# Optimization experiments

Measured on AMD Instinct MI355X. Metric: run time of the kernel, lower is better.

## Reference

```python
import jax, jax.numpy as jnp
import numpy as np
from jax import lax

# ---- config (mirrors init_kwargs) ----
B, CIN, T, WIDTH = 32, 8, 256, 128
COUT = 64
K = (5, 5)
PAD = (2, 2)            # ceil((k-1)*dilation/2) per dim
OUT_W = 128             # output_shape
EPS = 1e-8
BETA0 = 0.9             # beta 'constant' init, one_per_layer
B0 = 1.0                # b 'constant' init
SIGMA0 = 10.0
MAX_SPK = 3.0           # Max_spikes_per_run


@jax.custom_vjp
def spike_fn(mthr, sigma):
    # Surrogate Heaviside: hard threshold fwd, sigmoid-derivative surrogate bwd.
    return (mthr > 0).astype(mthr.dtype)

def _spike_fwd(mthr, sigma):
    return spike_fn(mthr, sigma), (mthr, sigma)

def _spike_bwd(res, g):
    mthr, sigma = res
    sg = jax.nn.sigmoid(sigma * mthr)
    return (g * sigma * sg * (1.0 - sg), jnp.zeros_like(sigma))

spike_fn.defvjp(_spike_fwd, _spike_bwd)


def setup_inputs() -> dict:
    key = jax.random.key(0)
    kx, kw = jax.random.split(key)
    x = jax.random.normal(kx, (B, CIN, T, WIDTH), dtype=jnp.float32)
    w_std = 1.0 * np.sqrt(1.0 / (CIN * K[0] * K[1]))
    w = jax.random.normal(kw, (COUT, CIN, K[0], K[1]), dtype=jnp.float32) * w_std
    b = jnp.full((COUT,), B0, dtype=jnp.float32)          # clamped >= 0
    beta = jnp.array([BETA0], dtype=jnp.float32)           # one_per_layer, clamped to [0,1]
    sigma = jnp.array([SIGMA0], dtype=jnp.float32)         # surrogate_sigma_mode 'one'
    return {"x": x, "w": w, "b": b, "beta": beta, "sigma": sigma}


def _forward(x, w, b, beta, sigma):
    # conv over (time, width) with 'same'-style padding, then truncate width
    conv_x = lax.conv_general_dilated(
        x, w, window_strides=(1, 1),
        padding=((PAD[0], PAD[0]), (PAD[1], PAD[1])),
        rhs_dilation=(1, 1),
        dimension_numbers=("NCHW", "OIHW", "NCHW"))
    conv_x = conv_x[:, :, :, :OUT_W]                      # [B, COUT, T, OUT_W]

    d = jnp.einsum("oikl,eikl->oe", w, w)                 # lateral matrix [COUT, COUT]
    norm = jnp.sum(w * w, axis=(1, 2, 3))                 # [COUT]
    inv_norm = 1.0 / (norm + EPS)
    beta_s = beta[0]

    conv_seq = jnp.transpose(conv_x, (2, 0, 1, 3))        # [T, B, COUT, OUT_W]

    def step(carry, inp_t):
        mem, spk, prev = carry
        rst = jnp.einsum("bcw,cd->bdw", spk, d)           # lateral reset
        # Leaky neuron, soft reset
        mem = (mem - rst) * beta_s + inp_t * (1.0 - beta_s)
        mthr = mem * inv_norm[None, :, None] - b[None, :, None]
        s = (MAX_SPK - prev) * spike_fn(mthr, sigma)      # spike_limit=True
        prev = prev + s
        return (mem, s, prev), s

    zeros = jnp.zeros((B, COUT, OUT_W), dtype=x.dtype)
    (_, _, _), spk_rec = lax.scan(step, (zeros, zeros, zeros), conv_seq)
    # spk_rec: [T, B, COUT, OUT_W]

    loss = 0.5 * jnp.mean(spk_rec ** 2)                   # 'squared'
    spk_spread = jnp.max(jnp.sum(spk_rec, axis=(1, 2, 3))) / (B * COUT * OUT_W)  # 'max'

    output = jnp.transpose(spk_rec, (1, 2, 0, 3))         # [B, COUT, T, OUT_W]
    return output, loss, spk_spread


def reference(x, w, b, beta, sigma):
    return _forward(x, w, b, beta, sigma)
```

## Files before the change

### kernel.cpp

```cpp
#include <hip/hip_runtime.h>
#include <cstdint>


#define NB 32
#define NC 8
#define NT 256
#define NW 128
#define NO 64
#define WT 16
#define TC 8
#define NROWS 12
#define NCHUNK (NT / TC)
#define WPITCH 324

__global__ __launch_bounds__(1024)
void prep_kernel(const float* __restrict__ w, float* __restrict__ d3,
                 float* __restrict__ invn, unsigned int* __restrict__ gfires)
{
    __shared__ float wsh[NO * 200];
    const int tid = threadIdx.x;
    for (int i = tid; i < NO * 200; i += 1024) wsh[i] = w[i];
    if (tid < NT) gfires[tid] = 0u;
    __syncthreads();
#pragma unroll
    for (int p = 0; p < 4; ++p) {
        int idx = p * 1024 + tid;
        int o = idx >> 6, e = idx & 63;
        float acc = 0.0f;
        for (int i = 0; i < 200; i += 4) {
            float4 av = *(const float4*)&wsh[o * 200 + i];
            float4 bv = *(const float4*)&wsh[e * 200 + i];
            acc += av.x * bv.x + av.y * bv.y + av.z * bv.z + av.w * bv.w;
        }
        d3[idx] = 3.0f * acc;
        if (o == e) invn[o] = 1.0f / (acc + 1e-8f);
    }
}

__global__ __launch_bounds__(256, 1)
void spk_kernel(const float* __restrict__ x, const float* __restrict__ wglob,
                const float* __restrict__ bias, const float* __restrict__ beta_p,
                const float* __restrict__ d3g, const float* __restrict__ invng,
                float* __restrict__ out, unsigned int* __restrict__ gfires)
{
    __shared__ float wsm[NO * WPITCH];
    __shared__ float d3s[NO * NO];
    __shared__ float xsh[NC][NROWS][20];
    __shared__ unsigned long long smask[3][WT];
    __shared__ unsigned int scnt[3];
    __shared__ unsigned int sfires[NT];

    const int tid = threadIdx.x;
    const int bb  = blockIdx.x >> 3;
    const int w0  = (blockIdx.x & 7) * WT;
    const int co  = tid >> 2;
    const int wq4 = (tid & 3) * 4;

    for (int i = tid; i < NO * 200; i += 256) {
        int oi = i / 200; int r = i - oi * 200; int g = r / 5; int kw = r - g * 5;
        wsm[oi * WPITCH + g * 8 + kw] = wglob[i];
    }
    for (int i = tid; i < NO * NO; i += 256) d3s[i] = d3g[i];
    if (tid < WT) { smask[0][tid] = 0ull; smask[1][tid] = 0ull; smask[2][tid] = 0ull; }
    if (tid < 3) scnt[tid] = 0u;
    sfires[tid] = 0u;

    const size_t xbbase = (size_t)bb * NC * NT * NW;
#pragma unroll
    for (int k = 0; k < 8; ++k) {
        int i = tid + k * 256;
        if (i < NC * NROWS * 20) {
            int c = i / (NROWS * 20); int rem = i - c * (NROWS * 20);
            int row = rem / 20; int col = rem - row * 20;
            int tg = row - 2; int wg = w0 + col - 2;
            float v = 0.0f;
            if (tg >= 0 && tg < NT && wg >= 0 && wg < NW)
                v = x[xbbase + ((size_t)c * NT + tg) * NW + wg];
            ((float*)xsh)[i] = v;
        }
    }

    const float invn = invng[co];
    const float bco  = bias[co];
    const float beta = beta_p[0];
    const float omb  = 1.0f - beta;

    float mem0 = 0.f, mem1 = 0.f, mem2 = 0.f, mem3 = 0.f;
    unsigned int fired = 0u;

    __syncthreads();

#pragma unroll 1
    for (int ch = 0; ch < NCHUNK; ++ch) {
        const int tbase = ch * TC;

        float sreg[8];
        if (ch + 1 < NCHUNK) {
#pragma unroll
            for (int k = 0; k < 8; ++k) {
                int i = tid + k * 256;
                sreg[k] = 0.0f;
                if (i < NC * NROWS * 20) {
                    int c = i / (NROWS * 20); int rem = i - c * (NROWS * 20);
                    int row = rem / 20; int col = rem - row * 20;
                    int tg = tbase + TC - 2 + row; int wg = w0 + col - 2;
                    if (tg >= 0 && tg < NT && wg >= 0 && wg < NW)
                        sreg[k] = x[xbbase + ((size_t)c * NT + tg) * NW + wg];
                }
            }
        }

        float acc[TC][4];
#pragma unroll
        for (int t = 0; t < TC; ++t) { acc[t][0] = acc[t][1] = acc[t][2] = acc[t][3] = 0.f; }

#pragma unroll 1
        for (int c = 0; c < NC; ++c) {
            float4 xr[NROWS][2];
#pragma unroll
            for (int r = 0; r < NROWS; ++r) {
                const float4* p = (const float4*)&xsh[c][r][wq4];
                xr[r][0] = p[0];
                xr[r][1] = p[1];
            }
            float4 wv0[5], wv1[5];
#pragma unroll
            for (int kt = 0; kt < 5; ++kt) {
                const float4* p = (const float4*)&wsm[co * WPITCH + (c * 5 + kt) * 8];
                wv0[kt] = p[0]; wv1[kt] = p[1];
            }
#pragma unroll
            for (int kt = 0; kt < 5; ++kt) {
                float4 wv = wv0[kt]; float w4 = wv1[kt].x;
#pragma unroll
                for (int t = 0; t < TC; ++t) {
                    float4 xa = xr[t + kt][0];
                    float4 xb = xr[t + kt][1];
                    acc[t][0] += wv.x * xa.x + wv.y * xa.y + wv.z * xa.z + wv.w * xa.w + w4 * xb.x;
                    acc[t][1] += wv.x * xa.y + wv.y * xa.z + wv.z * xa.w + wv.w * xb.x + w4 * xb.y;
                    acc[t][2] += wv.x * xa.z + wv.y * xa.w + wv.z * xb.x + wv.w * xb.y + w4 * xb.z;
                    acc[t][3] += wv.x * xa.w + wv.y * xb.x + wv.z * xb.y + wv.w * xb.z + w4 * xb.w;
                }
            }
        }

#pragma unroll
        for (int tt = 0; tt < TC; ++tt) {
            const int t = tbase + tt;
            const int cur = t % 3, nxt = (t + 1) % 3, clr = (t + 2) % 3;

            if (tid < WT) smask[clr][tid] = 0ull;
            if (tid == 0) scnt[clr] = 0u;

            float r0 = 0.f, r1 = 0.f, r2 = 0.f, r3 = 0.f;
            if (scnt[cur] != 0u) {
                unsigned long long m0 = smask[cur][wq4 + 0];
                unsigned long long m1 = smask[cur][wq4 + 1];
                unsigned long long m2 = smask[cur][wq4 + 2];
                unsigned long long m3 = smask[cur][wq4 + 3];
                while (m0) { int c = __builtin_ctzll(m0); m0 &= m0 - 1; r0 += d3s[c * NO + co]; }
                while (m1) { int c = __builtin_ctzll(m1); m1 &= m1 - 1; r1 += d3s[c * NO + co]; }
                while (m2) { int c = __builtin_ctzll(m2); m2 &= m2 - 1; r2 += d3s[c * NO + co]; }
                while (m3) { int c = __builtin_ctzll(m3); m3 &= m3 - 1; r3 += d3s[c * NO + co]; }
            }

            mem0 = (mem0 - r0) * beta + acc[tt][0] * omb;
            mem1 = (mem1 - r1) * beta + acc[tt][1] * omb;
            mem2 = (mem2 - r2) * beta + acc[tt][2] * omb;
            mem3 = (mem3 - r3) * beta + acc[tt][3] * omb;

            float s0 = 0.f, s1 = 0.f, s2 = 0.f, s3 = 0.f;
            if (!(fired & 1u) && (mem0 * invn - bco > 0.0f)) {
                s0 = 3.0f; fired |= 1u;
                atomicOr(&smask[nxt][wq4 + 0], 1ull << co);
                atomicAdd(&sfires[t], 1u); atomicAdd(&scnt[nxt], 1u);
            }
            if (!(fired & 2u) && (mem1 * invn - bco > 0.0f)) {
                s1 = 3.0f; fired |= 2u;
                atomicOr(&smask[nxt][wq4 + 1], 1ull << co);
                atomicAdd(&sfires[t], 1u); atomicAdd(&scnt[nxt], 1u);
            }
            if (!(fired & 4u) && (mem2 * invn - bco > 0.0f)) {
                s2 = 3.0f; fired |= 4u;
                atomicOr(&smask[nxt][wq4 + 2], 1ull << co);
                atomicAdd(&sfires[t], 1u); atomicAdd(&scnt[nxt], 1u);
            }
            if (!(fired & 8u) && (mem3 * invn - bco > 0.0f)) {
                s3 = 3.0f; fired |= 8u;
                atomicOr(&smask[nxt][wq4 + 3], 1ull << co);
                atomicAdd(&sfires[t], 1u); atomicAdd(&scnt[nxt], 1u);
            }

            float4 sv = make_float4(s0, s1, s2, s3);
            *(float4*)(out + (((size_t)(bb * NO + co) * NT + t) * NW + w0 + wq4)) = sv;

            __syncthreads();
        }

        if (ch + 1 < NCHUNK) {
#pragma unroll
            for (int k = 0; k < 8; ++k) {
                int i = tid + k * 256;
                if (i < NC * NROWS * 20) ((float*)xsh)[i] = sreg[k];
            }
            __syncthreads();
        }
    }

    atomicAdd(&gfires[tid], sfires[tid]);
}

__global__ __launch_bounds__(256)
void fin_kernel(const unsigned int* __restrict__ gfires, float* __restrict__ out)
{
    const int tid = threadIdx.x;
    unsigned int v = gfires[tid];
    unsigned int s = v, m = v;
    for (int off = 32; off > 0; off >>= 1) {
        s += __shfl_down(s, off);
        unsigned int o = __shfl_down(m, off);
        m = m > o ? m : o;
    }
    __shared__ unsigned int ls[4], lm[4];
    if ((tid & 63) == 0) { ls[tid >> 6] = s; lm[tid >> 6] = m; }
    __syncthreads();
    if (tid == 0) {
        unsigned int ts = 0, tm = 0;
        for (int i = 0; i < 4; ++i) { ts += ls[i]; tm = tm > lm[i] ? tm : lm[i]; }
        out[67108864] = 4.5f * (float)ts / 67108864.0f;
        out[67108865] = 3.0f * (float)tm / 262144.0f;
    }
}

extern "C" void kernel_launch(void* const* d_in, const int* in_sizes, int n_in,
                              void* d_out, int out_size, void* d_ws, size_t ws_size,
                              hipStream_t stream)
{
    const float* x    = (const float*)d_in[0];
    const float* w    = (const float*)d_in[1];
    const float* b    = (const float*)d_in[2];
    const float* beta = (const float*)d_in[3];

    float* out  = (float*)d_out;
    float* wsf  = (float*)d_ws;
    float* d3   = wsf;
    float* invn = wsf + 4096;
    unsigned int* gf = (unsigned int*)(wsf + 4160);

    prep_kernel<<<1, 1024, 0, stream>>>(w, d3, invn, gf);
    spk_kernel<<<256, 256, 0, stream>>>(x, w, b, beta, d3, invn, out, gf);
    fin_kernel<<<1, 256, 0, stream>>>(gf, out);
}
```

Before: 823.3 us.

## Map channels to wave lanes, use ballot-based spike masks, defer output writes

Restructures the spiking kernel so each 64-lane wave owns all 64 output channels for two width columns. This lets the lateral reset masks be built with __ballot in registers instead of shared-memory atomics. The per-timestep block barrier is removed, leaving one sync per chunk, and the x tile is double-buffered. Spike times are packed as per-chunk codes in shared memory and written out as dense float4 stores one chunk later. Blocks grow to 512 threads with a two-blocks-per-CU bound, and the weight layout is transposed to be lane-contiguous. Register pressure changes, and memory writes become more coalesced.

```diff
diff --git a/kernel.cpp b/kernel.cpp
--- a/kernel.cpp
+++ b/kernel.cpp
@@ -11,7 +11,8 @@
 #define TC 8
 #define NROWS 12
 #define NCHUNK (NT / TC)
-#define WPITCH 324
+#define XCOLS 20
+#define XTILE (NC * NROWS * XCOLS)
 
 __global__ __launch_bounds__(1024)
 void prep_kernel(const float* __restrict__ w, float* __restrict__ d3,
@@ -37,177 +38,181 @@
     }
 }
 
-__global__ __launch_bounds__(256, 1)
+__global__ __launch_bounds__(512, 2)
 void spk_kernel(const float* __restrict__ x, const float* __restrict__ wglob,
                 const float* __restrict__ bias, const float* __restrict__ beta_p,
                 const float* __restrict__ d3g, const float* __restrict__ invng,
                 float* __restrict__ out, unsigned int* __restrict__ gfires)
 {
-    __shared__ float wsm[NO * WPITCH];
+    __shared__ float wsm[NC * 25 * NO];
     __shared__ float d3s[NO * NO];
-    __shared__ float xsh[NC][NROWS][20];
-    __shared__ unsigned long long smask[3][WT];
-    __shared__ unsigned int scnt[3];
-    __shared__ unsigned int sfires[NT];
-
-    const int tid = threadIdx.x;
-    const int bb  = blockIdx.x >> 3;
-    const int w0  = (blockIdx.x & 7) * WT;
-    const int co  = tid >> 2;
-    const int wq4 = (tid & 3) * 4;
-
-    for (int i = tid; i < NO * 200; i += 256) {
-        int oi = i / 200; int r = i - oi * 200; int g = r / 5; int kw = r - g * 5;
-        wsm[oi * WPITCH + g * 8 + kw] = wglob[i];
-    }
-    for (int i = tid; i < NO * NO; i += 256) d3s[i] = d3g[i];
-    if (tid < WT) { smask[0][tid] = 0ull; smask[1][tid] = 0ull; smask[2][tid] = 0ull; }
-    if (tid < 3) scnt[tid] = 0u;
-    sfires[tid] = 0u;
+    __shared__ float xsh[2][NC][NROWS][XCOLS];
+    __shared__ unsigned short tf[2][NO][8];
+    __shared__ unsigned int sf[NT];
+
+    const int tid  = threadIdx.x;
+    const int lane = tid & 63;
+    const int wv   = tid >> 6;
+    const int bb   = blockIdx.x >> 3;
+    const int w0   = (blockIdx.x & 7) * WT;
+
+    for (int i = tid; i < NC * 25 * NO; i += 512) {
+        int co = i & 63; int r = i >> 6;
+        int kw = r % 5; int r2 = r / 5; int kt = r2 % 5; int c = r2 / 5;
+        wsm[i] = wglob[((co * NC + c) * 5 + kt) * 5 + kw];
+    }
+    for (int i = tid; i < NO * NO; i += 512) d3s[i] = d3g[i];
+    for (int i = tid; i < NT; i += 512) sf[i] = 0u;
 
     const size_t xbbase = (size_t)bb * NC * NT * NW;
 #pragma unroll
-    for (int k = 0; k < 8; ++k) {
-        int i = tid + k * 256;
-        if (i < NC * NROWS * 20) {
-            int c = i / (NROWS * 20); int rem = i - c * (NROWS * 20);
-            int row = rem / 20; int col = rem - row * 20;
-            int tg = row - 2; int wg = w0 + col - 2;
+    for (int k = 0; k < 4; ++k) {
+        int i = tid + k * 512;
+        if (i < XTILE) {
+            int c = i / (NROWS * XCOLS); int rem = i - c * (NROWS * XCOLS);
+            int row = rem / XCOLS; int col = rem - row * XCOLS;
+            int tg = row - 2, wg = w0 + col - 2;
             float v = 0.0f;
             if (tg >= 0 && tg < NT && wg >= 0 && wg < NW)
                 v = x[xbbase + ((size_t)c * NT + tg) * NW + wg];
-            ((float*)xsh)[i] = v;
-        }
-    }
-
-    const float invn = invng[co];
-    const float bco  = bias[co];
+            (&xsh[0][0][0][0])[i] = v;
+        }
+    }
+
+    const float invn = invng[lane];
+    const float bco  = bias[lane];
     const float beta = beta_p[0];
     const float omb  = 1.0f - beta;
 
-    float mem0 = 0.f, mem1 = 0.f, mem2 = 0.f, mem3 = 0.f;
+    float mem0 = 0.f, mem1 = 0.f;
     unsigned int fired = 0u;
+    unsigned long long pm0 = 0ull, pm1 = 0ull;
+
+    const int sq = tid & 3;
+    const int srow = tid >> 2;
 
     __syncthreads();
 
 #pragma unroll 1
     for (int ch = 0; ch < NCHUNK; ++ch) {
+        const int buf = ch & 1;
         const int tbase = ch * TC;
 
-        float sreg[8];
+        float sr0 = 0.f, sr1 = 0.f, sr2 = 0.f, sr3 = 0.f;
         if (ch + 1 < NCHUNK) {
 #pragma unroll
-            for (int k = 0; k < 8; ++k) {
-                int i = tid + k * 256;
-                sreg[k] = 0.0f;
-                if (i < NC * NROWS * 20) {
-                    int c = i / (NROWS * 20); int rem = i - c * (NROWS * 20);
-                    int row = rem / 20; int col = rem - row * 20;
-                    int tg = tbase + TC - 2 + row; int wg = w0 + col - 2;
-                    if (tg >= 0 && tg < NT && wg >= 0 && wg < NW)
-                        sreg[k] = x[xbbase + ((size_t)c * NT + tg) * NW + wg];
+            for (int k = 0; k < 4; ++k) {
+                int i = tid + k * 512;
+                float v = 0.0f;
+                if (i < XTILE) {
+                    int c = i / (NROWS * XCOLS); int rem = i - c * (NROWS * XCOLS);
+                    int row = rem / XCOLS; int col = rem - row * XCOLS;
+                    int tg = tbase + 6 + row, wg = w0 + col - 2;
+                    if (tg < NT && wg >= 0 && wg < NW)
+                        v = x[xbbase + ((size_t)c * NT + tg) * NW + wg];
                 }
-            }
-        }
-
-        float acc[TC][4];
-#pragma unroll
-        for (int t = 0; t < TC; ++t) { acc[t][0] = acc[t][1] = acc[t][2] = acc[t][3] = 0.f; }
+                if (k == 0) sr0 = v; else if (k == 1) sr1 = v;
+                else if (k == 2) sr2 = v; else sr3 = v;
+            }
+        }
+
+        if (ch > 0) {
+            const int pbuf = buf ^ 1;
+            const int tprev = tbase - TC;
+#pragma unroll
+            for (int p = 0; p < 4; ++p) {
+                int rowi = p * 128 + srow;
+                int co = rowi >> 3, tt = rowi & 7;
+                unsigned int codes = *(const unsigned int*)&tf[pbuf][co][sq * 2];
+                float4 v;
+                v.x = (((codes      ) & 0xffu) == (unsigned)tt) ? 3.0f : 0.0f;
+                v.y = (((codes >>  8) & 0xffu) == (unsigned)tt) ? 3.0f : 0.0f;
+                v.z = (((codes >> 16) & 0xffu) == (unsigned)tt) ? 3.0f : 0.0f;
+                v.w = (((codes >> 24) & 0xffu) == (unsigned)tt) ? 3.0f : 0.0f;
+                *(float4*)(out + (((size_t)(bb * NO + co) * NT + tprev + tt) * NW + w0 + sq * 4)) = v;
+            }
+        }
+
+        float acc[TC][2];
+#pragma unroll
+        for (int t = 0; t < TC; ++t) { acc[t][0] = 0.f; acc[t][1] = 0.f; }
 
 #pragma unroll 1
         for (int c = 0; c < NC; ++c) {
-            float4 xr[NROWS][2];
+            float2 xr[NROWS][3];
 #pragma unroll
             for (int r = 0; r < NROWS; ++r) {
-                const float4* p = (const float4*)&xsh[c][r][wq4];
-                xr[r][0] = p[0];
-                xr[r][1] = p[1];
-            }
-            float4 wv0[5], wv1[5];
+                const float* base = &xsh[buf][c][r][2 * wv];
+                xr[r][0] = *(const float2*)(base);
+                xr[r][1] = *(const float2*)(base + 2);
+                xr[r][2] = *(const float2*)(base + 4);
+            }
 #pragma unroll
             for (int kt = 0; kt < 5; ++kt) {
-                const float4* p = (const float4*)&wsm[co * WPITCH + (c * 5 + kt) * 8];
-                wv0[kt] = p[0]; wv1[kt] = p[1];
-            }
-#pragma unroll
-            for (int kt = 0; kt < 5; ++kt) {
-                float4 wv = wv0[kt]; float w4 = wv1[kt].x;
+                const float* wp = &wsm[((c * 5 + kt) * 5) * 64 + lane];
+                float wk0 = wp[0], wk1 = wp[64], wk2 = wp[128], wk3 = wp[192], wk4 = wp[256];
 #pragma unroll
                 for (int t = 0; t < TC; ++t) {
-                    float4 xa = xr[t + kt][0];
-                    float4 xb = xr[t + kt][1];
-                    acc[t][0] += wv.x * xa.x + wv.y * xa.y + wv.z * xa.z + wv.w * xa.w + w4 * xb.x;
-                    acc[t][1] += wv.x * xa.y + wv.y * xa.z + wv.z * xa.w + wv.w * xb.x + w4 * xb.y;
-                    acc[t][2] += wv.x * xa.z + wv.y * xa.w + wv.z * xb.x + wv.w * xb.y + w4 * xb.z;
-                    acc[t][3] += wv.x * xa.w + wv.y * xb.x + wv.z * xb.y + wv.w * xb.z + w4 * xb.w;
+                    float2 a = xr[t + kt][0], b2 = xr[t + kt][1], c2 = xr[t + kt][2];
+                    acc[t][0] += wk0 * a.x + wk1 * a.y + wk2 * b2.x + wk3 * b2.y + wk4 * c2.x;
+                    acc[t][1] += wk0 * a.y + wk1 * b2.x + wk2 * b2.y + wk3 * c2.x + wk4 * c2.y;
                 }
             }
         }
 
+        unsigned int tfc0 = 0xffu, tfc1 = 0xffu;
 #pragma unroll
         for (int tt = 0; tt < TC; ++tt) {
-            const int t = tbase + tt;
-            const int cur = t % 3, nxt = (t + 1) % 3, clr = (t + 2) % 3;
-
-            if (tid < WT) smask[clr][tid] = 0ull;
-            if (tid == 0) scnt[clr] = 0u;
-
-            float r0 = 0.f, r1 = 0.f, r2 = 0.f, r3 = 0.f;
-            if (scnt[cur] != 0u) {
-                unsigned long long m0 = smask[cur][wq4 + 0];
-                unsigned long long m1 = smask[cur][wq4 + 1];
-                unsigned long long m2 = smask[cur][wq4 + 2];
-                unsigned long long m3 = smask[cur][wq4 + 3];
-                while (m0) { int c = __builtin_ctzll(m0); m0 &= m0 - 1; r0 += d3s[c * NO + co]; }
-                while (m1) { int c = __builtin_ctzll(m1); m1 &= m1 - 1; r1 += d3s[c * NO + co]; }
-                while (m2) { int c = __builtin_ctzll(m2); m2 &= m2 - 1; r2 += d3s[c * NO + co]; }
-                while (m3) { int c = __builtin_ctzll(m3); m3 &= m3 - 1; r3 += d3s[c * NO + co]; }
-            }
-
+            float r0 = 0.f, r1 = 0.f;
+            if (pm0 | pm1) {
+                unsigned long long m = pm0;
+                while (m) { int c = __builtin_ctzll(m); m &= m - 1; r0 += d3s[c * 64 + lane]; }
+                m = pm1;
+                while (m) { int c = __builtin_ctzll(m); m &= m - 1; r1 += d3s[c * 64 + lane]; }
+            }
             mem0 = (mem0 - r0) * beta + acc[tt][0] * omb;
             mem1 = (mem1 - r1) * beta + acc[tt][1] * omb;
-            mem2 = (mem2 - r2) * beta + acc[tt][2] * omb;
-            mem3 = (mem3 - r3) * beta + acc[tt][3] * omb;
-
-            float s0 = 0.f, s1 = 0.f, s2 = 0.f, s3 = 0.f;
-            if (!(fired & 1u) && (mem0 * invn - bco > 0.0f)) {
-                s0 = 3.0f; fired |= 1u;
-                atomicOr(&smask[nxt][wq4 + 0], 1ull << co);
-                atomicAdd(&sfires[t], 1u); atomicAdd(&scnt[nxt], 1u);
-            }
-            if (!(fired & 2u) && (mem1 * invn - bco > 0.0f)) {
-                s1 = 3.0f; fired |= 2u;
-                atomicOr(&smask[nxt][wq4 + 1], 1ull << co);
-                atomicAdd(&sfires[t], 1u); atomicAdd(&scnt[nxt], 1u);
-            }
-            if (!(fired & 4u) && (mem2 * invn - bco > 0.0f)) {
-                s2 = 3.0f; fired |= 4u;
-                atomicOr(&smask[nxt][wq4 + 2], 1ull << co);
-                atomicAdd(&sfires[t], 1u); atomicAdd(&scnt[nxt], 1u);
-            }
-            if (!(fired & 8u) && (mem3 * invn - bco > 0.0f)) {
-                s3 = 3.0f; fired |= 8u;
-                atomicOr(&smask[nxt][wq4 + 3], 1ull << co);
-                atomicAdd(&sfires[t], 1u); atomicAdd(&scnt[nxt], 1u);
-            }
-
-            float4 sv = make_float4(s0, s1, s2, s3);
-            *(float4*)(out + (((size_t)(bb * NO + co) * NT + t) * NW + w0 + wq4)) = sv;
-
-            __syncthreads();
-        }
+            bool f0 = !(fired & 1u) && (mem0 * invn - bco > 0.0f);
+            bool f1 = !(fired & 2u) && (mem1 * invn - bco > 0.0f);
+            pm0 = __ballot(f0);
+            pm1 = __ballot(f1);
+            if (f0) { fired |= 1u; tfc0 = (unsigned)tt; }
+            if (f1) { fired |= 2u; tfc1 = (unsigned)tt; }
+            unsigned int cnt = (unsigned)(__popcll(pm0) + __popcll(pm1));
+            if (lane == 0 && cnt) atomicAdd(&sf[tbase + tt], cnt);
+        }
+        tf[buf][lane][wv] = (unsigned short)(tfc0 | (tfc1 << 8));
 
         if (ch + 1 < NCHUNK) {
-#pragma unroll
-            for (int k = 0; k < 8; ++k) {
-                int i = tid + k * 256;
-                if (i < NC * NROWS * 20) ((float*)xsh)[i] = sreg[k];
-            }
-            __syncthreads();
-        }
-    }
-
-    atomicAdd(&gfires[tid], sfires[tid]);
+            float* dst = &xsh[buf ^ 1][0][0][0];
+#pragma unroll
+            for (int k = 0; k < 4; ++k) {
+                int i = tid + k * 512;
+                float v = (k == 0) ? sr0 : (k == 1) ? sr1 : (k == 2) ? sr2 : sr3;
+                if (i < XTILE) dst[i] = v;
+            }
+        }
+        __syncthreads();
+    }
+
+    {
+        const int pbuf = (NCHUNK - 1) & 1;
+        const int tprev = NT - TC;
+#pragma unroll
+        for (int p = 0; p < 4; ++p) {
+            int rowi = p * 128 + srow;
+            int co = rowi >> 3, tt = rowi & 7;
+            unsigned int codes = *(const unsigned int*)&tf[pbuf][co][sq * 2];
+            float4 v;
+            v.x = (((codes      ) & 0xffu) == (unsigned)tt) ? 3.0f : 0.0f;
+            v.y = (((codes >>  8) & 0xffu) == (unsigned)tt) ? 3.0f : 0.0f;
+            v.z = (((codes >> 16) & 0xffu) == (unsigned)tt) ? 3.0f : 0.0f;
+            v.w = (((codes >> 24) & 0xffu) == (unsigned)tt) ? 3.0f : 0.0f;
+            *(float4*)(out + (((size_t)(bb * NO + co) * NT + tprev + tt) * NW + w0 + sq * 4)) = v;
+        }
+    }
+
+    if (tid < NT) atomicAdd(&gfires[tid], sf[tid]);
 }
 
 __global__ __launch_bounds__(256)
@@ -248,6 +253,6 @@
     unsigned int* gf = (unsigned int*)(wsf + 4160);
 
     prep_kernel<<<1, 1024, 0, stream>>>(w, d3, invn, gf);
-    spk_kernel<<<256, 256, 0, stream>>>(x, w, b, beta, d3, invn, out, gf);
+    spk_kernel<<<256, 512, 0, stream>>>(x, w, b, beta, d3, invn, out, gf);
     fin_kernel<<<1, 256, 0, stream>>>(gf, out);
 }
```

Result: faster. 778.0 us (-5.5%).
